# Kernel tuning notes

Measured on AMD Instinct MI355X. Metric: run time of the kernel, lower is better.

The kernel has to match this reference:

```python
import jax, jax.numpy as jnp
import numpy as np

F = 128; K = 64; SR_CUT = 10.0
NB = 5; NRI = 3; NRA = 2; NRO = 1
N_ATOMS = 10000; N_PAIRS = 320000


def act(x):
    # shifted softplus: softplus(x) - log(2)
    return jax.nn.softplus(x) - jnp.log(2.0).astype(x.dtype)


def residual(x, W1, b1, W2, b2):
    # PhysNet residual: x + dense2(dense1(act(x))) with activation on dense1
    h = act(act(x) @ W1 + b1)
    return x + h @ W2 + b2


def cutoff_fn(D):
    x = D / SR_CUT
    x3 = x * x * x; x4 = x3 * x; x5 = x4 * x
    return jnp.where(x < 1.0, 1.0 - 6.0 * x5 + 15.0 * x4 - 10.0 * x3, 0.0)


def setup_inputs() -> dict:
    key = jax.random.key(0)
    ks = jax.random.split(key, 24)

    def nrm(k, shape, s=0.05):
        return (jax.random.normal(k, shape) * s).astype(jnp.float32)

    inp = {}
    inp["Z"] = jax.random.randint(ks[0], (N_ATOMS,), 1, 95)
    inp["R"] = (jax.random.normal(ks[1], (N_ATOMS, 3)) * 3.0).astype(jnp.float32)
    inp["idx_i"] = jax.random.randint(ks[2], (N_PAIRS,), 0, N_ATOMS)
    inp["idx_j"] = jax.random.randint(ks[3], (N_PAIRS,), 0, N_ATOMS)
    s3 = float(np.sqrt(3.0))
    inp["embeddings"] = jax.random.uniform(ks[4], (95, F), minval=-s3, maxval=s3).astype(jnp.float32)
    inp["rbf_centers"] = jnp.linspace(1.0, float(np.exp(-SR_CUT)), K).astype(jnp.float32)
    width = (0.5 / ((1.0 - float(np.exp(-SR_CUT))) / K)) ** 2
    inp["rbf_widths"] = jnp.full((K,), width, dtype=jnp.float32)
    inp["k2f_W"] = nrm(ks[5], (NB, K, F))
    inp["Wi"] = nrm(ks[6], (NB, F, F)); inp["bi"] = jnp.zeros((NB, F), jnp.float32)
    inp["Wj"] = nrm(ks[7], (NB, F, F)); inp["bj"] = jnp.zeros((NB, F), jnp.float32)
    inp["ri_W1"] = nrm(ks[8], (NB, NRI, F, F)); inp["ri_b1"] = jnp.zeros((NB, NRI, F), jnp.float32)
    inp["ri_W2"] = nrm(ks[9], (NB, NRI, F, F)); inp["ri_b2"] = jnp.zeros((NB, NRI, F), jnp.float32)
    inp["dW"] = nrm(ks[10], (NB, F, F)); inp["db"] = jnp.zeros((NB, F), jnp.float32)
    inp["u"] = jnp.ones((NB, F), jnp.float32)
    inp["ra_W1"] = nrm(ks[11], (NB, NRA, F, F)); inp["ra_b1"] = jnp.zeros((NB, NRA, F), jnp.float32)
    inp["ra_W2"] = nrm(ks[12], (NB, NRA, F, F)); inp["ra_b2"] = jnp.zeros((NB, NRA, F), jnp.float32)
    inp["ro_W1"] = nrm(ks[13], (NB, NRO, F, F)); inp["ro_b1"] = jnp.zeros((NB, NRO, F), jnp.float32)
    inp["ro_W2"] = nrm(ks[14], (NB, NRO, F, F)); inp["ro_b2"] = jnp.zeros((NB, NRO, F), jnp.float32)
    inp["out_W"] = nrm(ks[15], (NB, F, 2))
    inp["Escale"] = jnp.ones((95,), jnp.float32); inp["Eshift"] = jnp.zeros((95,), jnp.float32)
    inp["Qscale"] = jnp.ones((95,), jnp.float32); inp["Qshift"] = jnp.zeros((95,), jnp.float32)
    return inp


def reference(Z, R, idx_i, idx_j, embeddings, rbf_centers, rbf_widths, k2f_W, Wi, bi, Wj, bj,
              ri_W1, ri_b1, ri_W2, ri_b2, dW, db, u, ra_W1, ra_b1, ra_W2, ra_b2,
              ro_W1, ro_b1, ro_W2, ro_b2, out_W, Escale, Eshift, Qscale, Qshift):
    N = R.shape[0]
    # gather-based interatomic distances: gather -> sub -> sumsq -> relu -> sqrt
    dR = R[idx_i] - R[idx_j]                                   # [P,3]
    Dij = jnp.sqrt(jax.nn.relu(jnp.sum(dR * dR, axis=-1)))     # [P]
    # RBF expansion with smooth cutoff
    rbf = cutoff_fn(Dij)[:, None] * jnp.exp(-rbf_widths * (jnp.exp(-Dij)[:, None] - rbf_centers) ** 2)  # [P,K]
    x = embeddings[Z]                                          # [N,F]
    Ea = jnp.zeros((N,), x.dtype)
    Qa = jnp.zeros((N,), x.dtype)
    nhloss = jnp.zeros((), x.dtype)
    last2 = None
    for b in range(NB):
        # --- interaction layer ---
        g = rbf @ k2f_W[b]                                     # [P,F]
        xa = act(x)
        xi = act(xa @ Wi[b] + bi[b])                           # [N,F]
        xj_feat = act(xa @ Wj[b] + bj[b])                      # [N,F]
        msg = g * xj_feat[idx_j]                               # [P,F] gather + modulate
        m = xi + jax.ops.segment_sum(msg, idx_i, num_segments=N)
        for l in range(NRI):
            m = residual(m, ri_W1[b, l], ri_b1[b, l], ri_W2[b, l], ri_b2[b, l])
        m = act(m)
        x = u[b] * x + m @ dW[b] + db[b]
        for l in range(NRA):
            x = residual(x, ra_W1[b, l], ra_b1[b, l], ra_W2[b, l], ra_b2[b, l])
        # --- output block ---
        o = x
        for l in range(NRO):
            o = residual(o, ro_W1[b, l], ro_b1[b, l], ro_W2[b, l], ro_b2[b, l])
        out = act(o) @ out_W[b]                                # [N,2] -> (Ea, Qa)
        Ea = Ea + out[:, 0]
        Qa = Qa + out[:, 1]
        out2 = out * out
        if b > 0:
            nhloss = nhloss + jnp.mean(out2 / (out2 + last2 + 1e-7))
        last2 = out2
    Ea = Escale[Z] * Ea + Eshift[Z]
    Qa = Qscale[Z] * Qa + Qshift[Z]
    return Ea, Qa, Dij, nhloss
```

## Files before the change

### kernel.cpp

```cpp
#include <hip/hip_runtime.h>

typedef __attribute__((ext_vector_type(8))) short bfrag;
typedef __attribute__((ext_vector_type(4))) float ffrag;

__device__ __forceinline__ unsigned short f2b(float f){
  unsigned int u = __float_as_uint(f);
  return (unsigned short)((u + 0x7FFFu + ((u >> 16) & 1u)) >> 16);
}
__device__ __forceinline__ float actf(float v){
  float e = __builtin_amdgcn_exp2f(-fabsf(v)*1.44269504088896341f);
  return fmaxf(v, 0.f) + __builtin_amdgcn_logf(1.f + e)*0.69314718055994531f - 0.69314718055994531f;
}

__global__ __launch_bounds__(256) void k_zero(float* p, int n){
  int i = blockIdx.x*256 + threadIdx.x;
  if (i < n) p[i] = 0.f;
}

__global__ __launch_bounds__(256) void k_dij_count(
    const float* __restrict__ R, const int* __restrict__ idx_i, const int* __restrict__ idx_j,
    float* __restrict__ DijF, float* __restrict__ Dout, int* __restrict__ counts, int P){
  int p = blockIdx.x*256 + threadIdx.x;
  if (p >= P) return;
  int i = idx_i[p], j = idx_j[p];
  float dx = R[i*3+0] - R[j*3+0];
  float dy = R[i*3+1] - R[j*3+1];
  float dz = R[i*3+2] - R[j*3+2];
  float D = sqrtf(fmaxf(dx*dx + dy*dy + dz*dz, 0.f));
  DijF[p] = D;
  Dout[p] = D;
  atomicAdd(&counts[i], 1);
}

__global__ __launch_bounds__(256) void k_scanA(const int* __restrict__ counts,
    int* __restrict__ locEx, int* __restrict__ bsum, int N){
  __shared__ int buf[256];
  int tid = threadIdx.x, idx = blockIdx.x*256 + tid;
  int v = (idx < N) ? counts[idx] : 0;
  buf[tid] = v;
  __syncthreads();
  for (int off = 1; off < 256; off <<= 1){
    int t = (tid >= off) ? buf[tid-off] : 0;
    __syncthreads();
    buf[tid] += t;
    __syncthreads();
  }
  if (idx < N) locEx[idx] = buf[tid] - v;
  if (tid == 255) bsum[blockIdx.x] = buf[255];
}
__global__ __launch_bounds__(64) void k_scanB(int* __restrict__ bsum,
    int* __restrict__ boff, int nb){
  if (threadIdx.x == 0){
    int acc = 0;
    for (int i = 0; i < nb; ++i){ boff[i] = acc; acc += bsum[i]; }
    boff[nb] = acc;
  }
}
__global__ __launch_bounds__(256) void k_scanC(const int* __restrict__ locEx,
    const int* __restrict__ boff, int* __restrict__ starts, int* __restrict__ cursor,
    int N, int nb){
  int idx = blockIdx.x*256 + threadIdx.x;
  if (idx < N){
    int s = locEx[idx] + boff[blockIdx.x];
    starts[idx] = s; cursor[idx] = s;
  }
  if (idx == 0) starts[N] = boff[nb];
}

__global__ __launch_bounds__(256) void k_scatter(const int* __restrict__ idx_i,
    const int* __restrict__ idx_j, const float* __restrict__ DijF,
    int* __restrict__ cursor, int* __restrict__ i_s, int* __restrict__ j_s,
    float* __restrict__ D_s, int P){
  int p = blockIdx.x*256 + threadIdx.x;
  if (p >= P) return;
  int i = idx_i[p];
  int pos = atomicAdd(&cursor[i], 1);
  i_s[pos] = i;
  j_s[pos] = idx_j[p];
  D_s[pos] = DijF[p];
}

__global__ __launch_bounds__(256) void k_rbf(
    const float* __restrict__ D_s, const float* __restrict__ cent, const float* __restrict__ wid,
    unsigned short* __restrict__ rbf_s, int P){
  int gid = blockIdx.x*256 + threadIdx.x;
  if (gid >= P*64) return;
  int t = gid >> 6, k = gid & 63;
  float D = D_s[t];
  float xc = D * 0.1f;
  float cut = 0.f;
  if (xc < 1.f){
    float x3 = xc*xc*xc, x4 = x3*xc, x5 = x4*xc;
    cut = 1.f - 6.f*x5 + 15.f*x4 - 10.f*x3;
  }
  float tt = expf(-D) - cent[k];
  rbf_s[gid] = f2b(cut * expf(-wid[k]*tt*tt));
}

__global__ __launch_bounds__(256) void k_prep(const float* __restrict__ k2f,
    unsigned short* __restrict__ k2fP){
  int gid = blockIdx.x*256 + threadIdx.x;
  if (gid >= 5120) return;
  int l = gid & 63, fr = (gid >> 6) & 15, b = gid >> 10;
  int tile = fr >> 1, kh = fr & 1;
  const float* src = k2f + (size_t)b*64*128;
  int n = tile*16 + (l & 15);
  int kbase = kh*32 + (l >> 4)*8;
  ushort4 o0, o1;
  o0.x = f2b(src[(kbase+0)*128+n]); o0.y = f2b(src[(kbase+1)*128+n]);
  o0.z = f2b(src[(kbase+2)*128+n]); o0.w = f2b(src[(kbase+3)*128+n]);
  o1.x = f2b(src[(kbase+4)*128+n]); o1.y = f2b(src[(kbase+5)*128+n]);
  o1.z = f2b(src[(kbase+6)*128+n]); o1.w = f2b(src[(kbase+7)*128+n]);
  ushort4* dst = (ushort4*)(k2fP + (size_t)gid*8);
  dst[0] = o0; dst[1] = o1;
}

__global__ __launch_bounds__(256) void k_prepAll(
    const float* __restrict__ riW1, const float* __restrict__ riW2,
    const float* __restrict__ dW,   const float* __restrict__ raW1,
    const float* __restrict__ raW2, const float* __restrict__ roW1,
    const float* __restrict__ roW2, const float* __restrict__ Wi,
    const float* __restrict__ Wj,   unsigned short* __restrict__ WBall){
  int gid = blockIdx.x*256 + threadIdx.x;
  if (gid >= 75*2048) return;
  int i = gid >> 11, r = gid & 2047;
  const float* S;
  int slot;
  if (i < 15)      { S = riW1 + (size_t)i*16384;      slot = (i/3)*15 + 2*(i%3); }
  else if (i < 30) { int j=i-15; S = riW2 + (size_t)j*16384; slot = (j/3)*15 + 2*(j%3) + 1; }
  else if (i < 35) { int j=i-30; S = dW   + (size_t)j*16384; slot = j*15 + 6; }
  else if (i < 45) { int j=i-35; S = raW1 + (size_t)j*16384; slot = (j/2)*15 + 7 + 2*(j%2); }
  else if (i < 55) { int j=i-45; S = raW2 + (size_t)j*16384; slot = (j/2)*15 + 8 + 2*(j%2); }
  else if (i < 60) { int j=i-55; S = roW1 + (size_t)j*16384; slot = j*15 + 11; }
  else if (i < 65) { int j=i-60; S = roW2 + (size_t)j*16384; slot = j*15 + 12; }
  else if (i < 70) { int j=i-65; S = Wi   + (size_t)j*16384; slot = ((j==0)?4:(j-1))*15 + 13; }
  else             { int j=i-70; S = Wj   + (size_t)j*16384; slot = ((j==0)?4:(j-1))*15 + 14; }
  int fr = r >> 6, l = r & 63;
  int T = fr >> 2, k0 = fr & 3;
  int n = T*16 + (l & 15);
  int kbase = k0*32 + (l >> 4)*8;
  unsigned short* D = WBall + ((size_t)slot*2048 + r)*8;
  ushort4 o0, o1;
  o0.x=f2b(S[(kbase+0)*128+n]); o0.y=f2b(S[(kbase+1)*128+n]);
  o0.z=f2b(S[(kbase+2)*128+n]); o0.w=f2b(S[(kbase+3)*128+n]);
  o1.x=f2b(S[(kbase+4)*128+n]); o1.y=f2b(S[(kbase+5)*128+n]);
  o1.z=f2b(S[(kbase+6)*128+n]); o1.w=f2b(S[(kbase+7)*128+n]);
  ((ushort4*)D)[0]=o0; ((ushort4*)D)[1]=o1;
}

__global__ __launch_bounds__(256) void k_prepO(const float* __restrict__ outW,
    unsigned short* __restrict__ outWB){
  int gid = blockIdx.x*256 + threadIdx.x;
  if (gid >= 5*256) return;
  int b = gid >> 8, r = gid & 255;
  int l = r & 63;
  int col = l & 15;
  int k0 = r >> 6;
  int kbase = k0*32 + (l >> 4)*8;
  ushort4 o0 = {0,0,0,0}, o1 = {0,0,0,0};
  if (col < 2){
    const float* S = outW + (size_t)b*256;
    o0.x=f2b(S[(kbase+0)*2+col]); o0.y=f2b(S[(kbase+1)*2+col]);
    o0.z=f2b(S[(kbase+2)*2+col]); o0.w=f2b(S[(kbase+3)*2+col]);
    o1.x=f2b(S[(kbase+4)*2+col]); o1.y=f2b(S[(kbase+5)*2+col]);
    o1.z=f2b(S[(kbase+6)*2+col]); o1.w=f2b(S[(kbase+7)*2+col]);
  }
  unsigned short* D = outWB + ((size_t)b*256 + r)*8;
  ((ushort4*)D)[0]=o0; ((ushort4*)D)[1]=o1;
}

__device__ __forceinline__ void mmtile(const unsigned short* tile,
    const unsigned short* __restrict__ WB, int w, int l, ffrag C[4]){
  int m = l & 15, q = l >> 4;
  bfrag A[4];
  #pragma unroll
  for (int k0 = 0; k0 < 4; ++k0)
    A[k0] = *(const bfrag*)(tile + m*136 + k0*32 + q*8);
  #pragma unroll
  for (int tt = 0; tt < 4; ++tt){
    ffrag c = {0.f,0.f,0.f,0.f};
    const bfrag* bp = (const bfrag*)(WB + (((w*4+tt)*4)*64 + l)*8);
    #pragma unroll
    for (int k0 = 0; k0 < 4; ++k0)
      c = __builtin_amdgcn_mfma_f32_16x16x32_bf16(A[k0], bp[k0*64], c, 0, 0, 0);
    C[tt] = c;
  }
}

__device__ __forceinline__ void loadB8(const unsigned short* __restrict__ WB,
    int w, int l, bfrag* B){
  #pragma unroll
  for (int tt = 0; tt < 2; ++tt)
    #pragma unroll
    for (int k0 = 0; k0 < 4; ++k0)
      B[tt*4+k0] = *(const bfrag*)(WB + ((size_t)((((w*2+tt)*4)+k0)*64 + l))*8);
}
__device__ __forceinline__ void mmB(const unsigned short* tile, const bfrag* B,
    int l, ffrag C[2]){
  int m = l & 15, q = l >> 4;
  bfrag A[4];
  #pragma unroll
  for (int k0 = 0; k0 < 4; ++k0)
    A[k0] = *(const bfrag*)(tile + m*136 + k0*32 + q*8);
  #pragma unroll
  for (int tt = 0; tt < 2; ++tt){
    ffrag c = {0.f,0.f,0.f,0.f};
    #pragma unroll
    for (int k0 = 0; k0 < 4; ++k0)
      c = __builtin_amdgcn_mfma_f32_16x16x32_bf16(A[k0], B[tt*4+k0], c, 0, 0, 0);
    C[tt] = c;
  }
}

__global__ __launch_bounds__(128) void k_phase1m(
    const int* __restrict__ Z, const float* __restrict__ emb,
    const unsigned short* __restrict__ WB45,
    const float* __restrict__ bi0, const float* __restrict__ bj0,
    float* __restrict__ x_g, float* __restrict__ m_g, float* __restrict__ xjb_g, int N){
  __shared__ unsigned short tile[16*136];
  int tid = threadIdx.x, w = tid >> 6, l = tid & 63;
  int m = l & 15, q = l >> 4, rbase = blockIdx.x*16;
  #pragma unroll
  for (int r = 0; r < 4; ++r){
    int row = rbase + q*4 + r;
    int z = Z[row];
    #pragma unroll
    for (int tt = 0; tt < 4; ++tt){
      int c = (w*4+tt)*16 + m;
      float v = emb[(size_t)z*128 + c];
      x_g[(size_t)row*128 + c] = v;
      tile[(q*4+r)*136 + c] = f2b(actf(v));
    }
  }
  __syncthreads();
  ffrag C[4];
  mmtile(tile, WB45 + 13*16384, w, l, C);
  #pragma unroll
  for (int tt = 0; tt < 4; ++tt){
    int c = (w*4+tt)*16 + m;
    float bb = bi0[c];
    #pragma unroll
    for (int r = 0; r < 4; ++r)
      m_g[(size_t)(rbase + q*4 + r)*128 + c] = actf(C[tt][r] + bb);
  }
  mmtile(tile, WB45 + 14*16384, w, l, C);
  #pragma unroll
  for (int tt = 0; tt < 4; ++tt){
    int c = (w*4+tt)*16 + m;
    float bb = bj0[c];
    #pragma unroll
    for (int r = 0; r < 4; ++r)
      xjb_g[(size_t)(rbase + q*4 + r)*128 + c] = actf(C[tt][r] + bb);
  }
}

__global__ __launch_bounds__(256) void k_pairmsg2(
    const unsigned short* __restrict__ rbf_s, const unsigned short* __restrict__ k2fP,
    const int* __restrict__ i_s, const int* __restrict__ j_s,
    const float* __restrict__ xj, float* __restrict__ m_g, int P){
  __shared__ float G[4][16*130];
  int tid = threadIdx.x, w = tid >> 6, l = tid & 63;
  float* Gw = &G[w][0];
  bfrag B[16];
  #pragma unroll
  for (int t = 0; t < 8; ++t){
    #pragma unroll
    for (int kh = 0; kh < 2; ++kh)
      B[t*2+kh] = *(const bfrag*)(k2fP + (size_t)((t*2+kh)*64 + l)*8);
  }
  int wstart = (blockIdx.x*4 + w)*128;
  if (wstart >= P) return;
  int row16 = l & 15, quad = l >> 4;
  float a0 = 0.f, a1 = 0.f;
  int iCur = -1;
  bfrag A0 = *(const bfrag*)(rbf_s + (size_t)(wstart + row16)*64 + quad*8);
  bfrag A1 = *(const bfrag*)(rbf_s + (size_t)(wstart + row16)*64 + 32 + quad*8);
  int4 iv[4], jv[4];
  #pragma unroll
  for (int g = 0; g < 4; ++g){
    iv[g] = *(const int4*)(i_s + wstart + g*4);
    jv[g] = *(const int4*)(j_s + wstart + g*4);
  }
  #pragma unroll 1
  for (int bi2 = 0; bi2 < 8; ++bi2){
    int bt = wstart + bi2*16;
    const int* ip = (const int*)iv;
    const int* jp = (const int*)jv;
    float2 xv[16];
    #pragma unroll
    for (int k = 0; k < 16; ++k)
      xv[k] = *(const float2*)(xj + (size_t)jp[k]*128 + 2*l);
    #pragma unroll
    for (int t = 0; t < 8; ++t){
      ffrag C = {0.f,0.f,0.f,0.f};
      C = __builtin_amdgcn_mfma_f32_16x16x32_bf16(A0, B[t*2],   C, 0, 0, 0);
      C = __builtin_amdgcn_mfma_f32_16x16x32_bf16(A1, B[t*2+1], C, 0, 0, 0);
      #pragma unroll
      for (int r = 0; r < 4; ++r)
        Gw[(quad*4+r)*130 + t*16 + row16] = C[r];
    }
    bfrag nA0, nA1;
    int4 niv[4], njv[4];
    if (bi2 < 7){
      int btn = bt + 16;
      nA0 = *(const bfrag*)(rbf_s + (size_t)(btn + row16)*64 + quad*8);
      nA1 = *(const bfrag*)(rbf_s + (size_t)(btn + row16)*64 + 32 + quad*8);
      #pragma unroll
      for (int g = 0; g < 4; ++g){
        niv[g] = *(const int4*)(i_s + btn + g*4);
        njv[g] = *(const int4*)(j_s + btn + g*4);
      }
    }
    #pragma unroll
    for (int k = 0; k < 16; ++k){
      int i = ip[k];
      if (i != iCur){
        if (iCur >= 0){
          unsafeAtomicAdd(&m_g[(size_t)iCur*128 + 2*l],     a0);
          unsafeAtomicAdd(&m_g[(size_t)iCur*128 + 2*l + 1], a1);
        }
        iCur = i; a0 = 0.f; a1 = 0.f;
      }
      float g0 = Gw[k*130 + 2*l], g1 = Gw[k*130 + 2*l + 1];
      a0 = fmaf(g0, xv[k].x, a0);
      a1 = fmaf(g1, xv[k].y, a1);
    }
    if (bi2 < 7){
      A0 = nA0; A1 = nA1;
      #pragma unroll
      for (int g = 0; g < 4; ++g){ iv[g] = niv[g]; jv[g] = njv[g]; }
    }
  }
  if (iCur >= 0){
    unsafeAtomicAdd(&m_g[(size_t)iCur*128 + 2*l],     a0);
    unsafeAtomicAdd(&m_g[(size_t)iCur*128 + 2*l + 1], a1);
  }
}

template<int HASNEXT, int NH>
__global__ __launch_bounds__(256) void k_phase2m(
    float* __restrict__ m_g, float* __restrict__ x_g, float* __restrict__ xjb_g,
    const unsigned short* __restrict__ WBb,
    const float* __restrict__ rib1, const float* __restrict__ rib2,
    const float* __restrict__ db, const float* __restrict__ u,
    const float* __restrict__ rab1, const float* __restrict__ rab2,
    const float* __restrict__ rob1, const float* __restrict__ rob2,
    const float* __restrict__ biN, const float* __restrict__ bjN,
    const unsigned short* __restrict__ outWBb,
    float* __restrict__ Ea, float* __restrict__ Qa,
    float* __restrict__ last2, float* __restrict__ nh, int N){
  __shared__ unsigned short tiles[2][16*136];
  __shared__ float biasS[16*128];
  int tid = threadIdx.x, w = tid >> 6, l = tid & 63;
  int m = l & 15, q = l >> 4, rbase = blockIdx.x*16;
  ffrag mC[2], xC[2], C[2];
  int cur = 0;
  const int nst = HASNEXT ? 15 : 13;
  const int slotSeq[15] = {0,1,2,3,4,5,6,7,8,9,10,
                           HASNEXT?13:11, HASNEXT?14:12, 11, 12};
  bfrag Bb[2][8];
  loadB8(WBb + (size_t)slotSeq[0]*16384, w, l, Bb[0]);

  if (tid < 128){
    biasS[0*128+tid]  = rib1[tid];
    biasS[1*128+tid]  = rib1[128+tid];
    biasS[2*128+tid]  = rib1[256+tid];
    biasS[3*128+tid]  = rib2[tid];
    biasS[4*128+tid]  = rib2[128+tid];
    biasS[5*128+tid]  = rib2[256+tid];
    biasS[6*128+tid]  = db[tid];
    biasS[7*128+tid]  = u[tid];
    biasS[8*128+tid]  = rab1[tid];
    biasS[9*128+tid]  = rab1[128+tid];
    biasS[10*128+tid] = rab2[tid];
    biasS[11*128+tid] = rab2[128+tid];
    biasS[12*128+tid] = rob1[tid];
    biasS[13*128+tid] = rob2[tid];
    biasS[14*128+tid] = biN[tid];
    biasS[15*128+tid] = bjN[tid];
  }
  float xrow[2][4];
  #pragma unroll
  for (int tt = 0; tt < 2; ++tt){
    int c = (w*2+tt)*16 + m;
    #pragma unroll
    for (int r = 0; r < 4; ++r)
      xrow[tt][r] = x_g[(size_t)(rbase + q*4 + r)*128 + c];
  }
  #pragma unroll
  for (int tt = 0; tt < 2; ++tt){
    int c = (w*2+tt)*16 + m;
    #pragma unroll
    for (int r = 0; r < 4; ++r){
      float v = m_g[(size_t)(rbase + q*4 + r)*128 + c];
      mC[tt][r] = v;
      tiles[0][(q*4+r)*136 + c] = f2b(actf(v));
    }
  }
  #pragma unroll
  for (int s = 0; s < nst; ++s){
    __syncthreads();
    if (s+1 < nst) loadB8(WBb + (size_t)slotSeq[s+1]*16384, w, l, Bb[(s+1)&1]);
    mmB(tiles[cur], Bb[s&1], l, C);
    if (HASNEXT && s == 11){
      #pragma unroll
      for (int tt = 0; tt < 2; ++tt){
        int c = (w*2+tt)*16 + m;
        float bb = biasS[14*128 + c];
        #pragma unroll
        for (int r = 0; r < 4; ++r)
          m_g[(size_t)(rbase + q*4 + r)*128 + c] = actf(C[tt][r] + bb);
      }
    } else if (HASNEXT && s == 12){
      #pragma unroll
      for (int tt = 0; tt < 2; ++tt){
        int c = (w*2+tt)*16 + m;
        float bb = biasS[15*128 + c];
        #pragma unroll
        for (int r = 0; r < 4; ++r)
          xjb_g[(size_t)(rbase + q*4 + r)*128 + c] = actf(C[tt][r] + bb);
      }
    } else if (s == 6){
      #pragma unroll
      for (int tt = 0; tt < 2; ++tt){
        int c = (w*2+tt)*16 + m;
        float uu = biasS[7*128 + c], bb = biasS[6*128 + c];
        #pragma unroll
        for (int r = 0; r < 4; ++r){
          float nv = uu*xrow[tt][r] + C[tt][r] + bb;
          xC[tt][r] = nv;
          tiles[1-cur][(q*4+r)*136 + c] = f2b(actf(nv));
        }
      }
      cur ^= 1;
    } else if (s == 1 || s == 3 || s == 5){
      #pragma unroll
      for (int tt = 0; tt < 2; ++tt){
        int c = (w*2+tt)*16 + m;
        float bb = biasS[(3 + (s>>1))*128 + c];
        #pragma unroll
        for (int r = 0; r < 4; ++r){
          float nv = mC[tt][r] + C[tt][r] + bb;
          mC[tt][r] = nv;
          tiles[1-cur][(q*4+r)*136 + c] = f2b(actf(nv));
        }
      }
      cur ^= 1;
    } else if (s == 8 || s == 10){
      #pragma unroll
      for (int tt = 0; tt < 2; ++tt){
        int c = (w*2+tt)*16 + m;
        float bb = biasS[(10 + ((s-8)>>1))*128 + c];
        #pragma unroll
        for (int r = 0; r < 4; ++r){
          float nv = xC[tt][r] + C[tt][r] + bb;
          xC[tt][r] = nv;
          tiles[1-cur][(q*4+r)*136 + c] = f2b(actf(nv));
          if (HASNEXT && s == 10)
            x_g[(size_t)(rbase + q*4 + r)*128 + c] = nv;
        }
      }
      cur ^= 1;
    } else if ((HASNEXT && s == 14) || (!HASNEXT && s == 12)){
      #pragma unroll
      for (int tt = 0; tt < 2; ++tt){
        int c = (w*2+tt)*16 + m;
        float bb = biasS[13*128 + c];
        #pragma unroll
        for (int r = 0; r < 4; ++r){
          float ov = xC[tt][r] + C[tt][r] + bb;
          tiles[1-cur][(q*4+r)*136 + c] = f2b(actf(ov));
        }
      }
      cur ^= 1;
    } else {
      int bidx = (s==0)?0:(s==2)?1:(s==4)?2:(s==7)?8:(s==9)?9:12;
      #pragma unroll
      for (int tt = 0; tt < 2; ++tt){
        int c = (w*2+tt)*16 + m;
        float bb = biasS[bidx*128 + c];
        #pragma unroll
        for (int r = 0; r < 4; ++r)
          tiles[1-cur][(q*4+r)*136 + c] = f2b(actf(C[tt][r] + bb));
      }
      cur ^= 1;
    }
  }
  __syncthreads();
  if (w == 0){
    bfrag A[4];
    #pragma unroll
    for (int k0 = 0; k0 < 4; ++k0)
      A[k0] = *(const bfrag*)(&tiles[cur][0] + m*136 + k0*32 + q*8);
    ffrag Ch = {0.f,0.f,0.f,0.f};
    #pragma unroll
    for (int k0 = 0; k0 < 4; ++k0){
      bfrag B = *(const bfrag*)(outWBb + (size_t)(k0*64 + l)*8);
      Ch = __builtin_amdgcn_mfma_f32_16x16x32_bf16(A[k0], B, Ch, 0, 0, 0);
    }
    int col = m;
    if (col < 2){
      float tp = 0.f;
      #pragma unroll
      for (int r = 0; r < 4; ++r){
        int row = rbase + q*4 + r;
        float val = Ch[r];
        if (col == 0) Ea[row] += val; else Qa[row] += val;
        float sq = val*val;
        if (NH){
          float lastv = last2[row*2 + col];
          tp += sq/(sq + lastv + 1e-7f);
        }
        last2[row*2 + col] = sq;
      }
      if (NH) unsafeAtomicAdd(nh, tp);
    }
  }
}

__global__ __launch_bounds__(256) void k_final(
    const int* __restrict__ Z, const float* __restrict__ Ea, const float* __restrict__ Qa,
    const float* __restrict__ Es, const float* __restrict__ Eh,
    const float* __restrict__ Qs, const float* __restrict__ Qh,
    const float* __restrict__ nh, float* __restrict__ out, int N, int P){
  int n = blockIdx.x*256 + threadIdx.x;
  if (n < N){
    int z = Z[n];
    out[n]   = Es[z]*Ea[n] + Eh[z];
    out[N+n] = Qs[z]*Qa[n] + Qh[z];
  }
  if (blockIdx.x == 0 && threadIdx.x == 0)
    out[(size_t)2*N + P] = nh[0] / (2.f * (float)N);
}

extern "C" void kernel_launch(void* const* d_in, const int* in_sizes, int n_in,
                              void* d_out, int out_size, void* d_ws, size_t ws_size,
                              hipStream_t stream){
  const int N = in_sizes[0];
  const int P = in_sizes[2];
  const int F = 128;

  const int* Z      = (const int*)d_in[0];
  const float* R    = (const float*)d_in[1];
  const int* idx_i  = (const int*)d_in[2];
  const int* idx_j  = (const int*)d_in[3];
  const float* emb  = (const float*)d_in[4];
  const float* cent = (const float*)d_in[5];
  const float* wid  = (const float*)d_in[6];
  const float* k2f  = (const float*)d_in[7];
  const float* Wi   = (const float*)d_in[8];  const float* bi   = (const float*)d_in[9];
  const float* Wj   = (const float*)d_in[10]; const float* bj   = (const float*)d_in[11];
  const float* riW1 = (const float*)d_in[12]; const float* rib1 = (const float*)d_in[13];
  const float* riW2 = (const float*)d_in[14]; const float* rib2 = (const float*)d_in[15];
  const float* dWp  = (const float*)d_in[16]; const float* dbp  = (const float*)d_in[17];
  const float* u    = (const float*)d_in[18];
  const float* raW1 = (const float*)d_in[19]; const float* rab1 = (const float*)d_in[20];
  const float* raW2 = (const float*)d_in[21]; const float* rab2 = (const float*)d_in[22];
  const float* roW1 = (const float*)d_in[23]; const float* rob1 = (const float*)d_in[24];
  const float* roW2 = (const float*)d_in[25]; const float* rob2 = (const float*)d_in[26];
  const float* outW = (const float*)d_in[27];
  const float* Es   = (const float*)d_in[28]; const float* Eh   = (const float*)d_in[29];
  const float* Qs   = (const float*)d_in[30]; const float* Qh   = (const float*)d_in[31];

  char* ws = (char*)d_ws;
  size_t off = 0;
  float* DijF  = (float*)(ws + off); off += (size_t)P*4;
  float* D_s   = (float*)(ws + off); off += (size_t)P*4;
  int*   i_s   = (int*)  (ws + off); off += (size_t)P*4;
  int*   j_s   = (int*)  (ws + off); off += (size_t)P*4;
  unsigned short* rbf_s = (unsigned short*)(ws + off); off += (size_t)P*64*2;
  unsigned short* k2fP  = (unsigned short*)(ws + off); off += (size_t)5*16*64*8*2;
  unsigned short* WBall = (unsigned short*)(ws + off); off += (size_t)75*16384*2;
  unsigned short* outWB = (unsigned short*)(ws + off); off += (size_t)5*2048*2;
  float* x     = (float*)(ws + off); off += (size_t)N*F*4;
  float* xjb   = (float*)(ws + off); off += (size_t)N*F*4;
  float* m     = (float*)(ws + off); off += (size_t)N*F*4;
  float* last2 = (float*)(ws + off); off += (size_t)N*2*4;
  float* Ea    = (float*)(ws + off); off += (size_t)N*4;
  float* Qa    = (float*)(ws + off); off += (size_t)N*4;
  float* nh    = (float*)(ws + off); off += 256;
  int*   counts= (int*)  (ws + off); off += (size_t)N*4;
  int*   starts= (int*)  (ws + off); off += (size_t)(N+1)*4;
  int*   cursor= (int*)  (ws + off); off += (size_t)N*4;
  int*   locEx = (int*)  (ws + off); off += (size_t)N*4;
  int*   bsum  = (int*)  (ws + off); off += 64*4;
  int*   boff  = (int*)  (ws + off); off += 68*4;

  float* outF = (float*)d_out;
  float* Dout = outF + (size_t)2*N;

  const int nb = (N + 255)/256;
  const int nzero = 3*N + 64;
  k_zero<<<dim3((nzero+255)/256), dim3(256), 0, stream>>>(Ea, nzero);
  k_dij_count<<<dim3((P+255)/256), dim3(256), 0, stream>>>(R, idx_i, idx_j, DijF, Dout, counts, P);
  k_scanA<<<dim3(nb), dim3(256), 0, stream>>>(counts, locEx, bsum, N);
  k_scanB<<<dim3(1), dim3(64), 0, stream>>>(bsum, boff, nb);
  k_scanC<<<dim3(nb), dim3(256), 0, stream>>>(locEx, boff, starts, cursor, N, nb);
  k_scatter<<<dim3((P+255)/256), dim3(256), 0, stream>>>(idx_i, idx_j, DijF, cursor, i_s, j_s, D_s, P);
  k_rbf<<<dim3((P*64+255)/256), dim3(256), 0, stream>>>(D_s, cent, wid, rbf_s, P);
  k_prep<<<dim3(20), dim3(256), 0, stream>>>(k2f, k2fP);
  k_prepAll<<<dim3((75*2048+255)/256), dim3(256), 0, stream>>>(riW1, riW2, dWp, raW1, raW2,
                                                               roW1, roW2, Wi, Wj, WBall);
  k_prepO<<<dim3(5), dim3(256), 0, stream>>>(outW, outWB);

  const int G16 = (N + 15)/16;
  k_phase1m<<<dim3(G16), dim3(128), 0, stream>>>(Z, emb, WBall + (size_t)4*15*16384,
                                                 bi, bj, x, m, xjb, N);

  const int pmg = (P + 511)/512;
  for (int b = 0; b < 5; ++b){
    k_pairmsg2<<<dim3(pmg), dim3(256), 0, stream>>>(rbf_s, k2fP + (size_t)b*16*64*8,
                                                    i_s, j_s, xjb, m, P);
    const unsigned short* WBb = WBall + (size_t)b*15*16384;
    const float* a_rib1 = rib1 + (size_t)b*3*F;
    const float* a_rib2 = rib2 + (size_t)b*3*F;
    const float* a_db   = dbp  + (size_t)b*F;
    const float* a_u    = u    + (size_t)b*F;
    const float* a_rab1 = rab1 + (size_t)b*2*F;
    const float* a_rab2 = rab2 + (size_t)b*2*F;
    const float* a_rob1 = rob1 + (size_t)b*F;
    const float* a_rob2 = rob2 + (size_t)b*F;
    int bn = (b < 4) ? (b+1) : 0;
    const float* a_biN = bi + (size_t)bn*F;
    const float* a_bjN = bj + (size_t)bn*F;
    const unsigned short* oWB = outWB + (size_t)b*2048;
    if (b == 0){
      k_phase2m<1,0><<<dim3(G16), dim3(256), 0, stream>>>(m, x, xjb, WBb,
        a_rib1, a_rib2, a_db, a_u, a_rab1, a_rab2, a_rob1, a_rob2,
        a_biN, a_bjN, oWB, Ea, Qa, last2, nh, N);
    } else if (b < 4){
      k_phase2m<1,1><<<dim3(G16), dim3(256), 0, stream>>>(m, x, xjb, WBb,
        a_rib1, a_rib2, a_db, a_u, a_rab1, a_rab2, a_rob1, a_rob2,
        a_biN, a_bjN, oWB, Ea, Qa, last2, nh, N);
    } else {
      k_phase2m<0,1><<<dim3(G16), dim3(256), 0, stream>>>(m, x, xjb, WBb,
        a_rib1, a_rib2, a_db, a_u, a_rab1, a_rab2, a_rob1, a_rob2,
        a_biN, a_bjN, oWB, Ea, Qa, last2, nh, N);
    }
  }
  k_final<<<dim3((N+255)/256), dim3(256), 0, stream>>>(Z, Ea, Qa, Es, Eh, Qs, Qh, nh, outF, N, P);
}
```

Before: 518.9 us.

## Process 32 atom rows per block in phase2 to reuse weight fragments

The per-atom MLP chain kernel now handles two 16-row tiles per block, so each weight fragment loaded from global memory feeds two MFMA passes instead of one. The grid is halved and bounds guards are added for partial tiles. The double-buffered prefetch of the next weight slot is dropped in favour of a synchronous load per stage, which saves registers but exposes load latency. Fewer blocks (about 313) may leave CUs underused on a large GPU.

```diff
diff --git a/kernel.cpp b/kernel.cpp
--- a/kernel.cpp
+++ b/kernel.cpp
@@ -349,17 +349,16 @@
     const unsigned short* __restrict__ outWBb,
     float* __restrict__ Ea, float* __restrict__ Qa,
     float* __restrict__ last2, float* __restrict__ nh, int N){
-  __shared__ unsigned short tiles[2][16*136];
+  __shared__ unsigned short tiles[2][32*136];
   __shared__ float biasS[16*128];
   int tid = threadIdx.x, w = tid >> 6, l = tid & 63;
-  int m = l & 15, q = l >> 4, rbase = blockIdx.x*16;
-  ffrag mC[2], xC[2], C[2];
+  int m = l & 15, q = l >> 4, rbase = blockIdx.x*32;
+  ffrag mC[2][2], xC[2][2], C[2][2];
   int cur = 0;
   const int nst = HASNEXT ? 15 : 13;
   const int slotSeq[15] = {0,1,2,3,4,5,6,7,8,9,10,
                            HASNEXT?13:11, HASNEXT?14:12, 11, 12};
-  bfrag Bb[2][8];
-  loadB8(WBb + (size_t)slotSeq[0]*16384, w, l, Bb[0]);
+  bfrag Bb[8];
 
   if (tid < 128){
     biasS[0*128+tid]  = rib1[tid];
@@ -379,119 +378,153 @@
     biasS[14*128+tid] = biN[tid];
     biasS[15*128+tid] = bjN[tid];
   }
-  float xrow[2][4];
-  #pragma unroll
-  for (int tt = 0; tt < 2; ++tt){
-    int c = (w*2+tt)*16 + m;
-    #pragma unroll
-    for (int r = 0; r < 4; ++r)
-      xrow[tt][r] = x_g[(size_t)(rbase + q*4 + r)*128 + c];
-  }
-  #pragma unroll
-  for (int tt = 0; tt < 2; ++tt){
-    int c = (w*2+tt)*16 + m;
+  int rr[2][4];
+  #pragma unroll
+  for (int T = 0; T < 2; ++T)
     #pragma unroll
     for (int r = 0; r < 4; ++r){
-      float v = m_g[(size_t)(rbase + q*4 + r)*128 + c];
-      mC[tt][r] = v;
-      tiles[0][(q*4+r)*136 + c] = f2b(actf(v));
-    }
-  }
+      int row = rbase + T*16 + q*4 + r;
+      rr[T][r] = (row < N) ? row : (N-1);
+    }
+  float xrow[2][2][4];
+  #pragma unroll
+  for (int T = 0; T < 2; ++T)
+    #pragma unroll
+    for (int tt = 0; tt < 2; ++tt){
+      int c = (w*2+tt)*16 + m;
+      #pragma unroll
+      for (int r = 0; r < 4; ++r)
+        xrow[T][tt][r] = x_g[(size_t)rr[T][r]*128 + c];
+    }
+  #pragma unroll
+  for (int T = 0; T < 2; ++T)
+    #pragma unroll
+    for (int tt = 0; tt < 2; ++tt){
+      int c = (w*2+tt)*16 + m;
+      #pragma unroll
+      for (int r = 0; r < 4; ++r){
+        float v = m_g[(size_t)rr[T][r]*128 + c];
+        mC[T][tt][r] = v;
+        tiles[0][(T*16 + q*4 + r)*136 + c] = f2b(actf(v));
+      }
+    }
   #pragma unroll
   for (int s = 0; s < nst; ++s){
     __syncthreads();
-    if (s+1 < nst) loadB8(WBb + (size_t)slotSeq[s+1]*16384, w, l, Bb[(s+1)&1]);
-    mmB(tiles[cur], Bb[s&1], l, C);
+    loadB8(WBb + (size_t)slotSeq[s]*16384, w, l, Bb);
+    mmB(&tiles[cur][0],        Bb, l, C[0]);
+    mmB(&tiles[cur][16*136],   Bb, l, C[1]);
     if (HASNEXT && s == 11){
       #pragma unroll
-      for (int tt = 0; tt < 2; ++tt){
-        int c = (w*2+tt)*16 + m;
-        float bb = biasS[14*128 + c];
+      for (int T = 0; T < 2; ++T)
         #pragma unroll
-        for (int r = 0; r < 4; ++r)
-          m_g[(size_t)(rbase + q*4 + r)*128 + c] = actf(C[tt][r] + bb);
-      }
+        for (int tt = 0; tt < 2; ++tt){
+          int c = (w*2+tt)*16 + m;
+          float bb = biasS[14*128 + c];
+          #pragma unroll
+          for (int r = 0; r < 4; ++r){
+            int row = rbase + T*16 + q*4 + r;
+            if (row < N) m_g[(size_t)row*128 + c] = actf(C[T][tt][r] + bb);
+          }
+        }
     } else if (HASNEXT && s == 12){
       #pragma unroll
-      for (int tt = 0; tt < 2; ++tt){
-        int c = (w*2+tt)*16 + m;
-        float bb = biasS[15*128 + c];
+      for (int T = 0; T < 2; ++T)
         #pragma unroll
-        for (int r = 0; r < 4; ++r)
-          xjb_g[(size_t)(rbase + q*4 + r)*128 + c] = actf(C[tt][r] + bb);
-      }
+        for (int tt = 0; tt < 2; ++tt){
+          int c = (w*2+tt)*16 + m;
+          float bb = biasS[15*128 + c];
+          #pragma unroll
+          for (int r = 0; r < 4; ++r){
+            int row = rbase + T*16 + q*4 + r;
+            if (row < N) xjb_g[(size_t)row*128 + c] = actf(C[T][tt][r] + bb);
+          }
+        }
     } else if (s == 6){
       #pragma unroll
-      for (int tt = 0; tt < 2; ++tt){
-        int c = (w*2+tt)*16 + m;
-        float uu = biasS[7*128 + c], bb = biasS[6*128 + c];
+      for (int T = 0; T < 2; ++T)
         #pragma unroll
-        for (int r = 0; r < 4; ++r){
-          float nv = uu*xrow[tt][r] + C[tt][r] + bb;
-          xC[tt][r] = nv;
-          tiles[1-cur][(q*4+r)*136 + c] = f2b(actf(nv));
-        }
-      }
+        for (int tt = 0; tt < 2; ++tt){
+          int c = (w*2+tt)*16 + m;
+          float uu = biasS[7*128 + c], bb = biasS[6*128 + c];
+          #pragma unroll
+          for (int r = 0; r < 4; ++r){
+            float nv = uu*xrow[T][tt][r] + C[T][tt][r] + bb;
+            xC[T][tt][r] = nv;
+            tiles[1-cur][(T*16 + q*4 + r)*136 + c] = f2b(actf(nv));
+          }
+        }
       cur ^= 1;
     } else if (s == 1 || s == 3 || s == 5){
       #pragma unroll
-      for (int tt = 0; tt < 2; ++tt){
-        int c = (w*2+tt)*16 + m;
-        float bb = biasS[(3 + (s>>1))*128 + c];
+      for (int T = 0; T < 2; ++T)
         #pragma unroll
-        for (int r = 0; r < 4; ++r){
-          float nv = mC[tt][r] + C[tt][r] + bb;
-          mC[tt][r] = nv;
-          tiles[1-cur][(q*4+r)*136 + c] = f2b(actf(nv));
-        }
-      }
+        for (int tt = 0; tt < 2; ++tt){
+          int c = (w*2+tt)*16 + m;
+          float bb = biasS[(3 + (s>>1))*128 + c];
+          #pragma unroll
+          for (int r = 0; r < 4; ++r){
+            float nv = mC[T][tt][r] + C[T][tt][r] + bb;
+            mC[T][tt][r] = nv;
+            tiles[1-cur][(T*16 + q*4 + r)*136 + c] = f2b(actf(nv));
+          }
+        }
       cur ^= 1;
     } else if (s == 8 || s == 10){
       #pragma unroll
-      for (int tt = 0; tt < 2; ++tt){
-        int c = (w*2+tt)*16 + m;
-        float bb = biasS[(10 + ((s-8)>>1))*128 + c];
+      for (int T = 0; T < 2; ++T)
         #pragma unroll
-        for (int r = 0; r < 4; ++r){
-          float nv = xC[tt][r] + C[tt][r] + bb;
-          xC[tt][r] = nv;
-          tiles[1-cur][(q*4+r)*136 + c] = f2b(actf(nv));
-          if (HASNEXT && s == 10)
-            x_g[(size_t)(rbase + q*4 + r)*128 + c] = nv;
-        }
-      }
+        for (int tt = 0; tt < 2; ++tt){
+          int c = (w*2+tt)*16 + m;
+          float bb = biasS[(10 + ((s-8)>>1))*128 + c];
+          #pragma unroll
+          for (int r = 0; r < 4; ++r){
+            float nv = xC[T][tt][r] + C[T][tt][r] + bb;
+            xC[T][tt][r] = nv;
+            tiles[1-cur][(T*16 + q*4 + r)*136 + c] = f2b(actf(nv));
+            if (HASNEXT && s == 10){
+              int row = rbase + T*16 + q*4 + r;
+              if (row < N) x_g[(size_t)row*128 + c] = nv;
+            }
+          }
+        }
       cur ^= 1;
     } else if ((HASNEXT && s == 14) || (!HASNEXT && s == 12)){
       #pragma unroll
-      for (int tt = 0; tt < 2; ++tt){
-        int c = (w*2+tt)*16 + m;
-        float bb = biasS[13*128 + c];
+      for (int T = 0; T < 2; ++T)
         #pragma unroll
-        for (int r = 0; r < 4; ++r){
-          float ov = xC[tt][r] + C[tt][r] + bb;
-          tiles[1-cur][(q*4+r)*136 + c] = f2b(actf(ov));
-        }
-      }
+        for (int tt = 0; tt < 2; ++tt){
+          int c = (w*2+tt)*16 + m;
+          float bb = biasS[13*128 + c];
+          #pragma unroll
+          for (int r = 0; r < 4; ++r){
+            float ov = xC[T][tt][r] + C[T][tt][r] + bb;
+            tiles[1-cur][(T*16 + q*4 + r)*136 + c] = f2b(actf(ov));
+          }
+        }
       cur ^= 1;
     } else {
       int bidx = (s==0)?0:(s==2)?1:(s==4)?2:(s==7)?8:(s==9)?9:12;
       #pragma unroll
-      for (int tt = 0; tt < 2; ++tt){
-        int c = (w*2+tt)*16 + m;
-        float bb = biasS[bidx*128 + c];
+      for (int T = 0; T < 2; ++T)
         #pragma unroll
-        for (int r = 0; r < 4; ++r)
-          tiles[1-cur][(q*4+r)*136 + c] = f2b(actf(C[tt][r] + bb));
-      }
+        for (int tt = 0; tt < 2; ++tt){
+          int c = (w*2+tt)*16 + m;
+          float bb = biasS[bidx*128 + c];
+          #pragma unroll
+          for (int r = 0; r < 4; ++r)
+            tiles[1-cur][(T*16 + q*4 + r)*136 + c] = f2b(actf(C[T][tt][r] + bb));
+        }
       cur ^= 1;
     }
   }
   __syncthreads();
-  if (w == 0){
+  if (w < 2){
+    const unsigned short* tp = &tiles[cur][0] + w*16*136;
     bfrag A[4];
     #pragma unroll
     for (int k0 = 0; k0 < 4; ++k0)
-      A[k0] = *(const bfrag*)(&tiles[cur][0] + m*136 + k0*32 + q*8);
+      A[k0] = *(const bfrag*)(tp + m*136 + k0*32 + q*8);
     ffrag Ch = {0.f,0.f,0.f,0.f};
     #pragma unroll
     for (int k0 = 0; k0 < 4; ++k0){
@@ -500,20 +533,22 @@
     }
     int col = m;
     if (col < 2){
-      float tp = 0.f;
+      float tpv = 0.f;
       #pragma unroll
       for (int r = 0; r < 4; ++r){
-        int row = rbase + q*4 + r;
-        float val = Ch[r];
-        if (col == 0) Ea[row] += val; else Qa[row] += val;
-        float sq = val*val;
-        if (NH){
-          float lastv = last2[row*2 + col];
-          tp += sq/(sq + lastv + 1e-7f);
-        }
-        last2[row*2 + col] = sq;
+        int row = rbase + w*16 + q*4 + r;
+        if (row < N){
+          float val = Ch[r];
+          if (col == 0) Ea[row] += val; else Qa[row] += val;
+          float sq = val*val;
+          if (NH){
+            float lastv = last2[row*2 + col];
+            tpv += sq/(sq + lastv + 1e-7f);
+          }
+          last2[row*2 + col] = sq;
+        }
       }
-      if (NH) unsafeAtomicAdd(nh, tp);
+      if (NH) unsafeAtomicAdd(nh, tpv);
     }
   }
 }
@@ -604,6 +639,7 @@
   k_prepO<<<dim3(5), dim3(256), 0, stream>>>(outW, outWB);
 
   const int G16 = (N + 15)/16;
+  const int G32 = (N + 31)/32;
   k_phase1m<<<dim3(G16), dim3(128), 0, stream>>>(Z, emb, WBall + (size_t)4*15*16384,
                                                  bi, bj, x, m, xjb, N);
 
@@ -625,15 +661,15 @@
     const float* a_bjN = bj + (size_t)bn*F;
     const unsigned short* oWB = outWB + (size_t)b*2048;
     if (b == 0){
-      k_phase2m<1,0><<<dim3(G16), dim3(256), 0, stream>>>(m, x, xjb, WBb,
+      k_phase2m<1,0><<<dim3(G32), dim3(256), 0, stream>>>(m, x, xjb, WBb,
         a_rib1, a_rib2, a_db, a_u, a_rab1, a_rab2, a_rob1, a_rob2,
         a_biN, a_bjN, oWB, Ea, Qa, last2, nh, N);
     } else if (b < 4){
-      k_phase2m<1,1><<<dim3(G16), dim3(256), 0, stream>>>(m, x, xjb, WBb,
+      k_phase2m<1,1><<<dim3(G32), dim3(256), 0, stream>>>(m, x, xjb, WBb,
         a_rib1, a_rib2, a_db, a_u, a_rab1, a_rab2, a_rob1, a_rob2,
         a_biN, a_bjN, oWB, Ea, Qa, last2, nh, N);
     } else {
-      k_phase2m<0,1><<<dim3(G16), dim3(256), 0, stream>>>(m, x, xjb, WBb,
+      k_phase2m<0,1><<<dim3(G32), dim3(256), 0, stream>>>(m, x, xjb, WBb,
         a_rib1, a_rib2, a_db, a_u, a_rab1, a_rab2, a_rob1, a_rob2,
         a_biN, a_bjN, oWB, Ea, Qa, last2, nh, N);
     }
```

Result: slower. 582.0 us (+12.2%).

## Split phase2 dense chain across 8 waves, one 16-column tile per wave

Applied to the files above, without the earlier changes.

Doubles the phase2 block from 4 to 8 waves so each wave computes a single 16-column output tile instead of two, which halves per-wave MFMA work and register use. The software prefetch of the next layer's weight fragments into a double buffer is removed; each stage now loads its weights just after the barrier. The aim is more parallelism per 16-row block and lower register pressure. The cost is twice as many threads at each of the 15 barriers and exposed weight-load latency. The bias preload still uses only the first 128 threads, and the final output step still runs on wave 0 only.

```diff
diff --git a/kernel.cpp b/kernel.cpp
--- a/kernel.cpp
+++ b/kernel.cpp
@@ -187,29 +187,22 @@
   }
 }
 
-__device__ __forceinline__ void loadB8(const unsigned short* __restrict__ WB,
+__device__ __forceinline__ void loadB4(const unsigned short* __restrict__ WB,
     int w, int l, bfrag* B){
   #pragma unroll
-  for (int tt = 0; tt < 2; ++tt)
-    #pragma unroll
-    for (int k0 = 0; k0 < 4; ++k0)
-      B[tt*4+k0] = *(const bfrag*)(WB + ((size_t)((((w*2+tt)*4)+k0)*64 + l))*8);
-}
-__device__ __forceinline__ void mmB(const unsigned short* tile, const bfrag* B,
-    int l, ffrag C[2]){
+  for (int k0 = 0; k0 < 4; ++k0)
+    B[k0] = *(const bfrag*)(WB + ((size_t)((w*4+k0)*64 + l))*8);
+}
+__device__ __forceinline__ void mmB1(const unsigned short* tile, const bfrag* B,
+    int l, ffrag& C){
   int m = l & 15, q = l >> 4;
-  bfrag A[4];
-  #pragma unroll
-  for (int k0 = 0; k0 < 4; ++k0)
-    A[k0] = *(const bfrag*)(tile + m*136 + k0*32 + q*8);
-  #pragma unroll
-  for (int tt = 0; tt < 2; ++tt){
-    ffrag c = {0.f,0.f,0.f,0.f};
-    #pragma unroll
-    for (int k0 = 0; k0 < 4; ++k0)
-      c = __builtin_amdgcn_mfma_f32_16x16x32_bf16(A[k0], B[tt*4+k0], c, 0, 0, 0);
-    C[tt] = c;
-  }
+  ffrag c = {0.f,0.f,0.f,0.f};
+  #pragma unroll
+  for (int k0 = 0; k0 < 4; ++k0){
+    bfrag A = *(const bfrag*)(tile + m*136 + k0*32 + q*8);
+    c = __builtin_amdgcn_mfma_f32_16x16x32_bf16(A, B[k0], c, 0, 0, 0);
+  }
+  C = c;
 }
 
 __global__ __launch_bounds__(128) void k_phase1m(
@@ -338,7 +331,7 @@
 }
 
 template<int HASNEXT, int NH>
-__global__ __launch_bounds__(256) void k_phase2m(
+__global__ __launch_bounds__(512) void k_phase2m(
     float* __restrict__ m_g, float* __restrict__ x_g, float* __restrict__ xjb_g,
     const unsigned short* __restrict__ WBb,
     const float* __restrict__ rib1, const float* __restrict__ rib2,
@@ -353,13 +346,13 @@
   __shared__ float biasS[16*128];
   int tid = threadIdx.x, w = tid >> 6, l = tid & 63;
   int m = l & 15, q = l >> 4, rbase = blockIdx.x*16;
-  ffrag mC[2], xC[2], C[2];
+  int c = w*16 + m;
+  ffrag mC, xC, C;
   int cur = 0;
   const int nst = HASNEXT ? 15 : 13;
   const int slotSeq[15] = {0,1,2,3,4,5,6,7,8,9,10,
                            HASNEXT?13:11, HASNEXT?14:12, 11, 12};
-  bfrag Bb[2][8];
-  loadB8(WBb + (size_t)slotSeq[0]*16384, w, l, Bb[0]);
+  bfrag Bb[4];
 
   if (tid < 128){
     biasS[0*128+tid]  = rib1[tid];
@@ -379,110 +372,74 @@
     biasS[14*128+tid] = biN[tid];
     biasS[15*128+tid] = bjN[tid];
   }
-  float xrow[2][4];
-  #pragma unroll
-  for (int tt = 0; tt < 2; ++tt){
-    int c = (w*2+tt)*16 + m;
-    #pragma unroll
-    for (int r = 0; r < 4; ++r)
-      xrow[tt][r] = x_g[(size_t)(rbase + q*4 + r)*128 + c];
-  }
-  #pragma unroll
-  for (int tt = 0; tt < 2; ++tt){
-    int c = (w*2+tt)*16 + m;
-    #pragma unroll
-    for (int r = 0; r < 4; ++r){
-      float v = m_g[(size_t)(rbase + q*4 + r)*128 + c];
-      mC[tt][r] = v;
-      tiles[0][(q*4+r)*136 + c] = f2b(actf(v));
-    }
+  float xrow[4];
+  #pragma unroll
+  for (int r = 0; r < 4; ++r)
+    xrow[r] = x_g[(size_t)(rbase + q*4 + r)*128 + c];
+  #pragma unroll
+  for (int r = 0; r < 4; ++r){
+    float v = m_g[(size_t)(rbase + q*4 + r)*128 + c];
+    mC[r] = v;
+    tiles[0][(q*4+r)*136 + c] = f2b(actf(v));
   }
   #pragma unroll
   for (int s = 0; s < nst; ++s){
     __syncthreads();
-    if (s+1 < nst) loadB8(WBb + (size_t)slotSeq[s+1]*16384, w, l, Bb[(s+1)&1]);
-    mmB(tiles[cur], Bb[s&1], l, C);
+    loadB4(WBb + (size_t)slotSeq[s]*16384, w, l, Bb);
+    mmB1(tiles[cur], Bb, l, C);
     if (HASNEXT && s == 11){
-      #pragma unroll
-      for (int tt = 0; tt < 2; ++tt){
-        int c = (w*2+tt)*16 + m;
-        float bb = biasS[14*128 + c];
-        #pragma unroll
-        for (int r = 0; r < 4; ++r)
-          m_g[(size_t)(rbase + q*4 + r)*128 + c] = actf(C[tt][r] + bb);
-      }
+      float bb = biasS[14*128 + c];
+      #pragma unroll
+      for (int r = 0; r < 4; ++r)
+        m_g[(size_t)(rbase + q*4 + r)*128 + c] = actf(C[r] + bb);
     } else if (HASNEXT && s == 12){
-      #pragma unroll
-      for (int tt = 0; tt < 2; ++tt){
-        int c = (w*2+tt)*16 + m;
-        float bb = biasS[15*128 + c];
-        #pragma unroll
-        for (int r = 0; r < 4; ++r)
-          xjb_g[(size_t)(rbase + q*4 + r)*128 + c] = actf(C[tt][r] + bb);
-      }
+      float bb = biasS[15*128 + c];
+      #pragma unroll
+      for (int r = 0; r < 4; ++r)
+        xjb_g[(size_t)(rbase + q*4 + r)*128 + c] = actf(C[r] + bb);
     } else if (s == 6){
-      #pragma unroll
-      for (int tt = 0; tt < 2; ++tt){
-        int c = (w*2+tt)*16 + m;
-        float uu = biasS[7*128 + c], bb = biasS[6*128 + c];
-        #pragma unroll
-        for (int r = 0; r < 4; ++r){
-          float nv = uu*xrow[tt][r] + C[tt][r] + bb;
-          xC[tt][r] = nv;
-          tiles[1-cur][(q*4+r)*136 + c] = f2b(actf(nv));
-        }
+      float uu = biasS[7*128 + c], bb = biasS[6*128 + c];
+      #pragma unroll
+      for (int r = 0; r < 4; ++r){
+        float nv = uu*xrow[r] + C[r] + bb;
+        xC[r] = nv;
+        tiles[1-cur][(q*4+r)*136 + c] = f2b(actf(nv));
       }
       cur ^= 1;
     } else if (s == 1 || s == 3 || s == 5){
-      #pragma unroll
-      for (int tt = 0; tt < 2; ++tt){
-        int c = (w*2+tt)*16 + m;
-        float bb = biasS[(3 + (s>>1))*128 + c];
-        #pragma unroll
-        for (int r = 0; r < 4; ++r){
-          float nv = mC[tt][r] + C[tt][r] + bb;
-          mC[tt][r] = nv;
-          tiles[1-cur][(q*4+r)*136 + c] = f2b(actf(nv));
-        }
+      float bb = biasS[(3 + (s>>1))*128 + c];
+      #pragma unroll
+      for (int r = 0; r < 4; ++r){
+        float nv = mC[r] + C[r] + bb;
+        mC[r] = nv;
+        tiles[1-cur][(q*4+r)*136 + c] = f2b(actf(nv));
       }
       cur ^= 1;
     } else if (s == 8 || s == 10){
-      #pragma unroll
-      for (int tt = 0; tt < 2; ++tt){
-        int c = (w*2+tt)*16 + m;
-        float bb = biasS[(10 + ((s-8)>>1))*128 + c];
-        #pragma unroll
-        for (int r = 0; r < 4; ++r){
-          float nv = xC[tt][r] + C[tt][r] + bb;
-          xC[tt][r] = nv;
-          tiles[1-cur][(q*4+r)*136 + c] = f2b(actf(nv));
-          if (HASNEXT && s == 10)
-            x_g[(size_t)(rbase + q*4 + r)*128 + c] = nv;
-        }
+      float bb = biasS[(10 + ((s-8)>>1))*128 + c];
+      #pragma unroll
+      for (int r = 0; r < 4; ++r){
+        float nv = xC[r] + C[r] + bb;
+        xC[r] = nv;
+        tiles[1-cur][(q*4+r)*136 + c] = f2b(actf(nv));
+        if (HASNEXT && s == 10)
+          x_g[(size_t)(rbase + q*4 + r)*128 + c] = nv;
       }
       cur ^= 1;
     } else if ((HASNEXT && s == 14) || (!HASNEXT && s == 12)){
-      #pragma unroll
-      for (int tt = 0; tt < 2; ++tt){
-        int c = (w*2+tt)*16 + m;
-        float bb = biasS[13*128 + c];
-        #pragma unroll
-        for (int r = 0; r < 4; ++r){
-          float ov = xC[tt][r] + C[tt][r] + bb;
-          tiles[1-cur][(q*4+r)*136 + c] = f2b(actf(ov));
-        }
+      float bb = biasS[13*128 + c];
+      #pragma unroll
+      for (int r = 0; r < 4; ++r){
+        float ov = xC[r] + C[r] + bb;
+        tiles[1-cur][(q*4+r)*136 + c] = f2b(actf(ov));
       }
       cur ^= 1;
     } else {
       int bidx = (s==0)?0:(s==2)?1:(s==4)?2:(s==7)?8:(s==9)?9:12;
-      #pragma unroll
-      for (int tt = 0; tt < 2; ++tt){
-        int c = (w*2+tt)*16 + m;
-        float bb = biasS[bidx*128 + c];
-        #pragma unroll
-        for (int r = 0; r < 4; ++r)
-          tiles[1-cur][(q*4+r)*136 + c] = f2b(actf(C[tt][r] + bb));
-      }
+      float bb = biasS[bidx*128 + c];
+      #pragma unroll
+      for (int r = 0; r < 4; ++r)
+        tiles[1-cur][(q*4+r)*136 + c] = f2b(actf(C[r] + bb));
       cur ^= 1;
     }
   }
@@ -625,15 +582,15 @@
     const float* a_bjN = bj + (size_t)bn*F;
     const unsigned short* oWB = outWB + (size_t)b*2048;
     if (b == 0){
-      k_phase2m<1,0><<<dim3(G16), dim3(256), 0, stream>>>(m, x, xjb, WBb,
+      k_phase2m<1,0><<<dim3(G16), dim3(512), 0, stream>>>(m, x, xjb, WBb,
         a_rib1, a_rib2, a_db, a_u, a_rab1, a_rab2, a_rob1, a_rob2,
         a_biN, a_bjN, oWB, Ea, Qa, last2, nh, N);
     } else if (b < 4){
-      k_phase2m<1,1><<<dim3(G16), dim3(256), 0, stream>>>(m, x, xjb, WBb,
+      k_phase2m<1,1><<<dim3(G16), dim3(512), 0, stream>>>(m, x, xjb, WBb,
         a_rib1, a_rib2, a_db, a_u, a_rab1, a_rab2, a_rob1, a_rob2,
         a_biN, a_bjN, oWB, Ea, Qa, last2, nh, N);
     } else {
-      k_phase2m<0,1><<<dim3(G16), dim3(256), 0, stream>>>(m, x, xjb, WBb,
+      k_phase2m<0,1><<<dim3(G16), dim3(512), 0, stream>>>(m, x, xjb, WBb,
         a_rib1, a_rib2, a_db, a_u, a_rab1, a_rab2, a_rob1, a_rob2,
         a_biN, a_bjN, oWB, Ea, Qa, last2, nh, N);
     }
```

Result: slower. 548.8 us (+5.8%).
